# Optimization experiments

Hardware: AMD Instinct MI355X
Metric: run time of the kernel (lower is better)

Reference implementation:

```python
import jax, jax.numpy as jnp
import numpy as np

THETA = 10000.0
IDENTITY_WEIGHT = 0.5


def _rotary(x):
    """lucidrains RotaryEmbedding(dim=D//2).rotate_queries_or_keys(x).

    Rotates the first rot_dim = D//2 channels with interleaved pair rotation;
    remaining channels pass through unchanged. x: [B, S, D].
    """
    D = x.shape[-1]
    rot_dim = D // 2  # RotaryEmbedding(dim) rotates `dim` channels
    half = rot_dim // 2
    pos = jnp.arange(x.shape[-2], dtype=x.dtype)                      # [S]
    inv_freq = 1.0 / (THETA ** (jnp.arange(0, rot_dim, 2, dtype=x.dtype) / rot_dim))  # [half]
    freqs = pos[:, None] * inv_freq[None, :]                          # [S, half]
    freqs = jnp.repeat(freqs, 2, axis=-1)                             # [S, rot_dim] interleaved f0,f0,f1,f1,...
    cos, sin = jnp.cos(freqs), jnp.sin(freqs)
    xr, rest = x[..., :rot_dim], x[..., rot_dim:]
    x1, x2 = xr[..., 0::2], xr[..., 1::2]
    rot_half = jnp.stack([-x2, x1], axis=-1).reshape(xr.shape)        # interleaved rotate_half
    out = xr * cos + rot_half * sin
    return jnp.concatenate([out, rest], axis=-1)


def setup_inputs() -> dict:
    key = jax.random.key(0)
    kx, kw = jax.random.split(key)
    B, S, D = 4, 4096, 2048
    X = jax.random.normal(kx, (B, S, D), dtype=jnp.float32)
    W = jax.random.normal(kw, (D, 2 * D), dtype=jnp.float32) * (1.0 / np.sqrt(D))
    b = jnp.zeros((2 * D,), dtype=jnp.float32)
    return {"X": X, "W": W, "b": b}


def reference(X, W, b):
    D = X.shape[-1]
    KV = jnp.einsum('bsd,df->bsf', X, W) + b          # in_proj: [B, S, 2D]
    K, V = KV[..., :D], KV[..., D:]
    K, V = _rotary(K), _rotary(V)
    fm = jnp.cos                                       # feature_map
    A = jnp.sum(fm(K) * fm(V), axis=-2, keepdims=True)  # reduce over sequence -> [B, 1, D]
    A = (1.0 - IDENTITY_WEIGHT) * A + IDENTITY_WEIGHT
    return A * X
```

## Files before the change

### kernel.cpp

```cpp
#include <hip/hip_runtime.h>
#include <hip/hip_bf16.h>

typedef __attribute__((ext_vector_type(4)))  int   i32x4;
typedef __attribute__((ext_vector_type(8)))  int   i32x8;
typedef __attribute__((ext_vector_type(16))) float f32x16;

#define NEG_L2K (-0.025952563241307517f)

#define VMW(N) asm volatile("s_waitcnt vmcnt(" #N ")" ::: "memory")
#define SCHB() __builtin_amdgcn_sched_barrier(0)
#define SBAR() __builtin_amdgcn_s_barrier()

#define AS1 __attribute__((address_space(1)))
#define AS3 __attribute__((address_space(3)))

__device__ __forceinline__ unsigned int pk4_fp8(float a, float b, float c, float d) {
    unsigned int v = __builtin_amdgcn_cvt_pk_fp8_f32(a, b, 0, false);
    v = __builtin_amdgcn_cvt_pk_fp8_f32(c, d, v, true);
    return v;
}

__global__ __launch_bounds__(256) void prep_x_kernel(const float* __restrict__ X,
                                                     unsigned char* __restrict__ Xf,
                                                     float* __restrict__ A) {
    int g = blockIdx.x * 256 + threadIdx.x;
    if (g < 8192) A[g] = 0.0f;
    int tileid = g >> 9;
    int mtile  = tileid >> 5;
    int kt     = tileid & 31;
    int c      = g & 511;
    int s      = c >> 6;
    int lane   = c & 63;
    int row  = mtile * 128 + (s >> 1) * 32 + (lane & 31);
    int kcol = kt * 64 + (lane >> 5) * 32 + (s & 1) * 16;
    const float* src = X + (size_t)row * 2048 + kcol;
    float4 f0 = *(const float4*)(src);
    float4 f1 = *(const float4*)(src + 4);
    float4 f2 = *(const float4*)(src + 8);
    float4 f3 = *(const float4*)(src + 12);
    uint4 o;
    o.x = pk4_fp8(f0.x, f0.y, f0.z, f0.w);
    o.y = pk4_fp8(f1.x, f1.y, f1.z, f1.w);
    o.z = pk4_fp8(f2.x, f2.y, f2.z, f2.w);
    o.w = pk4_fp8(f3.x, f3.y, f3.z, f3.w);
    *(uint4*)(Xf + (size_t)g * 16) = o;
}

__global__ __launch_bounds__(256) void prep_w_kernel(const float* __restrict__ W,
                                                     unsigned char* __restrict__ Wf) {
    __shared__ unsigned char t[64][72];
    int f0 = blockIdx.x * 64;
    int k0 = blockIdx.y * 64;
    int tx = threadIdx.x & 63;
    int ty = threadIdx.x >> 6;
    for (int r = ty; r < 64; r += 4) {
        float w = W[(size_t)(k0 + r) * 4096 + f0 + tx] * 16.0f;
        t[r][tx] = (unsigned char)(__builtin_amdgcn_cvt_pk_fp8_f32(w, w, 0, false) & 0xFF);
    }
    __syncthreads();
    int c   = threadIdx.x;
    int il  = c & 31;
    int lh  = (c >> 5) & 1;
    int rd  = (c >> 6) & 1;
    int wcl = c >> 7;
    int col_l = wcl * 32 + il;
    int kl    = lh * 32 + rd * 16;
    int fh    = f0 & 2047;
    int KV    = f0 >> 11;
    int ntile = fh >> 7;
    int wcg   = ((fh >> 5) & 2) + wcl;
    union { unsigned char b[16]; uint4 v; } ob;
    #pragma unroll
    for (int b = 0; b < 16; ++b) ob.b[b] = t[kl + b][col_l];
    size_t base = ((((size_t)ntile * 32 + blockIdx.y) * 2 + KV) << 13)
                + (size_t)(((wcg * 2 + rd) * 64 + lh * 32 + il) << 4);
    *(uint4*)(Wf + base) = ob.v;
}

__global__ __launch_bounds__(256, 2) void gemm_acos_kernel(
    const unsigned char* __restrict__ Xf,
    const unsigned char* __restrict__ Wf,
    const float* __restrict__ bias,
    float* __restrict__ A)
{
    __shared__ __align__(16) unsigned char Als[2][8192];
    __shared__ __align__(16) unsigned char Kls[2][8192];
    __shared__ __align__(16) unsigned char Vls[2][8192];

    const int tid  = threadIdx.x;
    const int lane = tid & 63;
    const int wc   = tid >> 6;
    const int l31  = lane & 31;
    const int lh   = lane >> 5;

    const int orig  = blockIdx.x;
    const int wg    = (orig & 7) * 256 + (orig >> 3);
    const int mtile = wg & 127;
    const int ntile = wg >> 7;
    const int row0  = mtile * 128;
    const int n0    = ntile * 128;

    const unsigned char* XfT = Xf + ((size_t)(mtile * 32) << 13);
    const unsigned char* WfT = Wf + ((size_t)(ntile * 32) << 14);

    f32x16 accK[4] = {};
    f32x16 accV[4] = {};

    const int abase = lane * 16;
    const int bbase = (wc * 128 + lane) * 16;

    #define STAGE(T, NB)                                                                    \
        do {                                                                                \
            const unsigned char* ga = XfT + ((size_t)(T) << 13);                            \
            const unsigned char* gw = WfT + ((size_t)(T) << 14);                            \
            __builtin_amdgcn_global_load_lds((const AS1 void*)(ga + tid * 16),              \
                (AS3 void*)(Als[NB] + tid * 16), 16, 0, 0);                                 \
            __builtin_amdgcn_global_load_lds((const AS1 void*)(ga + 4096 + tid * 16),       \
                (AS3 void*)(Als[NB] + 4096 + tid * 16), 16, 0, 0);                          \
            __builtin_amdgcn_global_load_lds((const AS1 void*)(gw + tid * 16),              \
                (AS3 void*)(Kls[NB] + tid * 16), 16, 0, 0);                                 \
            __builtin_amdgcn_global_load_lds((const AS1 void*)(gw + 4096 + tid * 16),       \
                (AS3 void*)(Kls[NB] + 4096 + tid * 16), 16, 0, 0);                          \
            __builtin_amdgcn_global_load_lds((const AS1 void*)(gw + 8192 + tid * 16),       \
                (AS3 void*)(Vls[NB] + tid * 16), 16, 0, 0);                                 \
            __builtin_amdgcn_global_load_lds((const AS1 void*)(gw + 12288 + tid * 16),      \
                (AS3 void*)(Vls[NB] + 4096 + tid * 16), 16, 0, 0);                          \
        } while (0)

    STAGE(0, 0);

    #pragma unroll 1
    for (int it = 0; it < 16; ++it) {
        #pragma unroll
        for (int sub = 0; sub < 2; ++sub) {
            const int t = it * 2 + sub;
            const bool last = (t == 31);
            const unsigned char* As = Als[sub];
            const unsigned char* Ks = Kls[sub];
            const unsigned char* Vs = Vls[sub];

            if (!last) { STAGE(t + 1, sub ^ 1); VMW(6); } else { VMW(0); }
            SCHB();
            SBAR();

            i32x8 a8[4], bk8, bv8;
            #pragma unroll
            for (int mf = 0; mf < 4; ++mf) {
                i32x4 lo = *(const i32x4*)(As + abase + mf * 2048);
                i32x4 hi = *(const i32x4*)(As + abase + mf * 2048 + 1024);
                a8[mf] = __builtin_shufflevector(lo, hi, 0, 1, 2, 3, 4, 5, 6, 7);
            }
            {
                i32x4 lo = *(const i32x4*)(Ks + bbase);
                i32x4 hi = *(const i32x4*)(Ks + bbase + 1024);
                bk8 = __builtin_shufflevector(lo, hi, 0, 1, 2, 3, 4, 5, 6, 7);
            }
            __builtin_amdgcn_s_setprio(1);
            #pragma unroll
            for (int mf = 0; mf < 4; ++mf)
                accK[mf] = __builtin_amdgcn_mfma_scale_f32_32x32x64_f8f6f4(
                    a8[mf], bk8, accK[mf], 0, 0, 0, 0x7F7F7F7F, 0, 0x7B7B7B7B);
            __builtin_amdgcn_s_setprio(0);

            {
                i32x4 lo = *(const i32x4*)(Vs + bbase);
                i32x4 hi = *(const i32x4*)(Vs + bbase + 1024);
                bv8 = __builtin_shufflevector(lo, hi, 0, 1, 2, 3, 4, 5, 6, 7);
            }
            __builtin_amdgcn_s_setprio(1);
            #pragma unroll
            for (int mf = 0; mf < 4; ++mf)
                accV[mf] = __builtin_amdgcn_mfma_scale_f32_32x32x64_f8f6f4(
                    a8[mf], bv8, accV[mf], 0, 0, 0, 0x7F7F7F7F, 0, 0x7B7B7B7B);
            __builtin_amdgcn_s_setprio(0);
            SBAR();
        }
    }

    const int batch = row0 >> 12;
    const int c     = n0 + wc * 32 + l31;
    const float bK  = bias[c];
    const float bV  = bias[c + 2048];
    const bool rot  = (c < 1024);
    const float invf = exp2f((float)(c >> 1) * NEG_L2K);
    const float sgn  = (c & 1) ? 1.0f : -1.0f;
    const int sbase  = (row0 & 4095) + 4 * lh;

    float colsum = 0.0f;
    #pragma unroll
    for (int mf = 0; mf < 4; ++mf) {
        #pragma unroll
        for (int r = 0; r < 16; ++r) {
            const int srow = sbase + mf * 32 + (r & 3) + 8 * (r >> 2);
            float kv = accK[mf][r] + bK;
            float vv = accV[mf][r] + bV;
            float pk = __shfl_xor(kv, 1);
            float pv = __shfl_xor(vv, 1);
            float kr = kv, vr = vv;
            if (rot) {
                float sn, cs;
                __sincosf((float)srow * invf, &sn, &cs);
                float tt = sgn * sn;
                kr = kv * cs + pk * tt;
                vr = vv * cs + pv * tt;
            }
            colsum += __cosf(kr) * __cosf(vr);
        }
    }
    colsum += __shfl_xor(colsum, 32);
    if (lane < 32)
        atomicAdd(&A[batch * 2048 + c], colsum);
}

__global__ void scale_out_kernel(const float* __restrict__ X,
                                 const float* __restrict__ A,
                                 float* __restrict__ out, int n4) {
    int gid = blockIdx.x * blockDim.x + threadIdx.x;
    int stride = gridDim.x * blockDim.x;
    for (int i = gid; i < n4; i += stride) {
        int e0 = i * 4;
        int b  = e0 >> 23;
        int d  = e0 & 2047;
        float4 a4 = *(const float4*)(A + b * 2048 + d);
        float4 x4 = ((const float4*)X)[i];
        float4 o;
        o.x = (0.5f * a4.x + 0.5f) * x4.x;
        o.y = (0.5f * a4.y + 0.5f) * x4.y;
        o.z = (0.5f * a4.z + 0.5f) * x4.z;
        o.w = (0.5f * a4.w + 0.5f) * x4.w;
        ((float4*)out)[i] = o;
    }
}

extern "C" void kernel_launch(void* const* d_in, const int* in_sizes, int n_in,
                              void* d_out, int out_size, void* d_ws, size_t ws_size,
                              hipStream_t stream) {
    const float* X    = (const float*)d_in[0];
    const float* W    = (const float*)d_in[1];
    const float* bias = (const float*)d_in[2];
    float* out = (float*)d_out;

    const size_t szA  = 32768;
    const size_t szWf = (size_t)4096 * 2048;
    const size_t szXf = (size_t)16384 * 2048;

    char* ws = (char*)d_ws;
    float* A = (float*)ws;
    unsigned char* Wf;
    unsigned char* Xf;
    if (ws_size >= szA + szWf + szXf) {
        Wf = (unsigned char*)(ws + szA);
        Xf = (unsigned char*)(ws + szA + szWf);
    } else if (ws_size >= szA + szWf) {
        Wf = (unsigned char*)(ws + szA);
        Xf = (unsigned char*)d_out;
    } else {
        Xf = (unsigned char*)d_out;
        Wf = (unsigned char*)d_out + szXf;
    }

    prep_x_kernel<<<8192, 256, 0, stream>>>(X, Xf, A);
    prep_w_kernel<<<dim3(64, 32), 256, 0, stream>>>(W, Wf);
    gemm_acos_kernel<<<2048, 256, 0, stream>>>(Xf, Wf, bias, A);
    scale_out_kernel<<<2048, 256, 0, stream>>>(X, A, out, 16384 * 2048 / 4);
}
```

Measured before the change: 232.0 us.

## Split GEMM tile to 64 columns with separate K and V waves for occupancy

Halves the N tile per workgroup to 64 columns and launches twice as many blocks. Each pair of waves now computes only K or only V, which halves the accumulators per thread, and the launch bound is raised to three blocks per CU. The epilogue combines cos(K) and cos(V) by staging cos(K) in LDS, which adds a block-wide sync and some LDS traffic. The trade-off is that the A tile is now loaded twice as often overall.

```diff
diff --git a/kernel.cpp b/kernel.cpp
--- a/kernel.cpp
+++ b/kernel.cpp
@@ -77,54 +77,53 @@
     *(uint4*)(Wf + base) = ob.v;
 }
 
-__global__ __launch_bounds__(256, 2) void gemm_acos_kernel(
+__global__ __launch_bounds__(256, 3) void gemm_acos_kernel(
     const unsigned char* __restrict__ Xf,
     const unsigned char* __restrict__ Wf,
     const float* __restrict__ bias,
     float* __restrict__ A)
 {
-    __shared__ __align__(16) unsigned char Als[2][8192];
-    __shared__ __align__(16) unsigned char Kls[2][8192];
-    __shared__ __align__(16) unsigned char Vls[2][8192];
+    __shared__ __align__(16) unsigned char SMEM[32768];
+    unsigned char* Als0 = SMEM;
+    unsigned char* Kls0 = SMEM + 16384;
+    unsigned char* Vls0 = SMEM + 24576;
 
     const int tid  = threadIdx.x;
     const int lane = tid & 63;
-    const int wc   = tid >> 6;
+    const int wid  = tid >> 6;
+    const int kv   = wid >> 1;
+    const int ch   = wid & 1;
     const int l31  = lane & 31;
     const int lh   = lane >> 5;
 
     const int orig  = blockIdx.x;
-    const int wg    = (orig & 7) * 256 + (orig >> 3);
+    const int wg    = (orig & 7) * 512 + (orig >> 3);
     const int mtile = wg & 127;
-    const int ntile = wg >> 7;
+    const int nt64  = wg >> 7;
     const int row0  = mtile * 128;
-    const int n0    = ntile * 128;
+    const int n0    = nt64 * 64;
 
     const unsigned char* XfT = Xf + ((size_t)(mtile * 32) << 13);
-    const unsigned char* WfT = Wf + ((size_t)(ntile * 32) << 14);
-
-    f32x16 accK[4] = {};
-    f32x16 accV[4] = {};
+    const unsigned char* WfT = Wf + ((size_t)((nt64 >> 1) * 32) << 14);
+    const int subN = (nt64 & 1) * 4096;
+
+    f32x16 acc[4] = {};
 
     const int abase = lane * 16;
-    const int bbase = (wc * 128 + lane) * 16;
+    const int bbase = ch * 2048 + lane * 16;
 
     #define STAGE(T, NB)                                                                    \
         do {                                                                                \
             const unsigned char* ga = XfT + ((size_t)(T) << 13);                            \
-            const unsigned char* gw = WfT + ((size_t)(T) << 14);                            \
+            const unsigned char* gw = WfT + ((size_t)(T) << 14) + subN;                     \
             __builtin_amdgcn_global_load_lds((const AS1 void*)(ga + tid * 16),              \
-                (AS3 void*)(Als[NB] + tid * 16), 16, 0, 0);                                 \
+                (AS3 void*)(Als0 + (NB) * 8192 + tid * 16), 16, 0, 0);                      \
             __builtin_amdgcn_global_load_lds((const AS1 void*)(ga + 4096 + tid * 16),       \
-                (AS3 void*)(Als[NB] + 4096 + tid * 16), 16, 0, 0);                          \
+                (AS3 void*)(Als0 + (NB) * 8192 + 4096 + tid * 16), 16, 0, 0);               \
             __builtin_amdgcn_global_load_lds((const AS1 void*)(gw + tid * 16),              \
-                (AS3 void*)(Kls[NB] + tid * 16), 16, 0, 0);                                 \
-            __builtin_amdgcn_global_load_lds((const AS1 void*)(gw + 4096 + tid * 16),       \
-                (AS3 void*)(Kls[NB] + 4096 + tid * 16), 16, 0, 0);                          \
+                (AS3 void*)(Kls0 + (NB) * 4096 + tid * 16), 16, 0, 0);                      \
             __builtin_amdgcn_global_load_lds((const AS1 void*)(gw + 8192 + tid * 16),       \
-                (AS3 void*)(Vls[NB] + tid * 16), 16, 0, 0);                                 \
-            __builtin_amdgcn_global_load_lds((const AS1 void*)(gw + 12288 + tid * 16),      \
-                (AS3 void*)(Vls[NB] + 4096 + tid * 16), 16, 0, 0);                          \
+                (AS3 void*)(Vls0 + (NB) * 4096 + tid * 16), 16, 0, 0);                      \
         } while (0)
 
     STAGE(0, 0);
@@ -135,15 +134,14 @@
         for (int sub = 0; sub < 2; ++sub) {
             const int t = it * 2 + sub;
             const bool last = (t == 31);
-            const unsigned char* As = Als[sub];
-            const unsigned char* Ks = Kls[sub];
-            const unsigned char* Vs = Vls[sub];
-
-            if (!last) { STAGE(t + 1, sub ^ 1); VMW(6); } else { VMW(0); }
+            const unsigned char* As = Als0 + sub * 8192;
+            const unsigned char* Bs = (kv ? Vls0 : Kls0) + sub * 4096;
+
+            if (!last) { STAGE(t + 1, sub ^ 1); VMW(4); } else { VMW(0); }
             SCHB();
             SBAR();
 
-            i32x8 a8[4], bk8, bv8;
+            i32x8 a8[4], b8;
             #pragma unroll
             for (int mf = 0; mf < 4; ++mf) {
                 i32x4 lo = *(const i32x4*)(As + abase + mf * 2048);
@@ -151,65 +149,65 @@
                 a8[mf] = __builtin_shufflevector(lo, hi, 0, 1, 2, 3, 4, 5, 6, 7);
             }
             {
-                i32x4 lo = *(const i32x4*)(Ks + bbase);
-                i32x4 hi = *(const i32x4*)(Ks + bbase + 1024);
-                bk8 = __builtin_shufflevector(lo, hi, 0, 1, 2, 3, 4, 5, 6, 7);
+                i32x4 lo = *(const i32x4*)(Bs + bbase);
+                i32x4 hi = *(const i32x4*)(Bs + bbase + 1024);
+                b8 = __builtin_shufflevector(lo, hi, 0, 1, 2, 3, 4, 5, 6, 7);
             }
             __builtin_amdgcn_s_setprio(1);
             #pragma unroll
             for (int mf = 0; mf < 4; ++mf)
-                accK[mf] = __builtin_amdgcn_mfma_scale_f32_32x32x64_f8f6f4(
-                    a8[mf], bk8, accK[mf], 0, 0, 0, 0x7F7F7F7F, 0, 0x7B7B7B7B);
-            __builtin_amdgcn_s_setprio(0);
-
-            {
-                i32x4 lo = *(const i32x4*)(Vs + bbase);
-                i32x4 hi = *(const i32x4*)(Vs + bbase + 1024);
-                bv8 = __builtin_shufflevector(lo, hi, 0, 1, 2, 3, 4, 5, 6, 7);
-            }
-            __builtin_amdgcn_s_setprio(1);
-            #pragma unroll
-            for (int mf = 0; mf < 4; ++mf)
-                accV[mf] = __builtin_amdgcn_mfma_scale_f32_32x32x64_f8f6f4(
-                    a8[mf], bv8, accV[mf], 0, 0, 0, 0x7F7F7F7F, 0, 0x7B7B7B7B);
+                acc[mf] = __builtin_amdgcn_mfma_scale_f32_32x32x64_f8f6f4(
+                    a8[mf], b8, acc[mf], 0, 0, 0, 0x7F7F7F7F, 0, 0x7B7B7B7B);
             __builtin_amdgcn_s_setprio(0);
             SBAR();
         }
     }
 
     const int batch = row0 >> 12;
-    const int c     = n0 + wc * 32 + l31;
-    const float bK  = bias[c];
-    const float bV  = bias[c + 2048];
+    const int c     = n0 + ch * 32 + l31;
+    const float bb  = bias[c + kv * 2048];
     const bool rot  = (c < 1024);
     const float invf = exp2f((float)(c >> 1) * NEG_L2K);
     const float sgn  = (c & 1) ? 1.0f : -1.0f;
     const int sbase  = (row0 & 4095) + 4 * lh;
 
-    float colsum = 0.0f;
+    float* cosLds = (float*)SMEM;
+    __syncthreads();
+
+    float cs_arr[4][16];
     #pragma unroll
     for (int mf = 0; mf < 4; ++mf) {
         #pragma unroll
         for (int r = 0; r < 16; ++r) {
-            const int srow = sbase + mf * 32 + (r & 3) + 8 * (r >> 2);
-            float kv = accK[mf][r] + bK;
-            float vv = accV[mf][r] + bV;
-            float pk = __shfl_xor(kv, 1);
-            float pv = __shfl_xor(vv, 1);
-            float kr = kv, vr = vv;
+            const int rloc = mf * 32 + (r & 3) + 8 * (r >> 2) + 4 * lh;
+            float x  = acc[mf][r] + bb;
+            float px = __shfl_xor(x, 1);
+            float xr = x;
             if (rot) {
-                float sn, cs;
-                __sincosf((float)srow * invf, &sn, &cs);
-                float tt = sgn * sn;
-                kr = kv * cs + pk * tt;
-                vr = vv * cs + pv * tt;
-            }
-            colsum += __cosf(kr) * __cosf(vr);
+                float sn, cc;
+                __sincosf((float)(sbase - 4 * lh + rloc) * invf, &sn, &cc);
+                xr = x * cc + px * (sgn * sn);
+            }
+            cs_arr[mf][r] = __cosf(xr);
+            if (kv == 0)
+                cosLds[ch * 4096 + rloc * 32 + l31] = cs_arr[mf][r];
         }
     }
-    colsum += __shfl_xor(colsum, 32);
-    if (lane < 32)
-        atomicAdd(&A[batch * 2048 + c], colsum);
+    __syncthreads();
+    if (kv == 1) {
+        float colsum = 0.0f;
+        #pragma unroll
+        for (int mf = 0; mf < 4; ++mf) {
+            #pragma unroll
+            for (int r = 0; r < 16; ++r) {
+                const int rloc = mf * 32 + (r & 3) + 8 * (r >> 2) + 4 * lh;
+                colsum += cs_arr[mf][r] * cosLds[ch * 4096 + rloc * 32 + l31];
+            }
+        }
+        colsum += __shfl_xor(colsum, 32);
+        if (lane < 32)
+            atomicAdd(&A[batch * 2048 + c], colsum);
+    }
 }
 
 __global__ void scale_out_kernel(const float* __restrict__ X,
@@ -261,6 +259,6 @@
 
     prep_x_kernel<<<8192, 256, 0, stream>>>(X, Xf, A);
     prep_w_kernel<<<dim3(64, 32), 256, 0, stream>>>(W, Wf);
-    gemm_acos_kernel<<<2048, 256, 0, stream>>>(Xf, Wf, bias, A);
+    gemm_acos_kernel<<<4096, 256, 0, stream>>>(Xf, Wf, bias, A);
     scale_out_kernel<<<2048, 256, 0, stream>>>(X, A, out, 16384 * 2048 / 4);
 }
```

Result: slower. 269.9 us (+16.4%).

## Widen GEMM block tile to 256 output columns per K and V

Applied to the files above, without the earlier changes.

Each block now computes two adjacent 128-column N tiles, so each wave holds 2x the K and V accumulators and reuses each loaded A fragment across twice as many MFMAs. The grid halves to 1024 blocks, LDS per block grows to 80KB, and launch bounds drop to one block per CU's worth of occupancy. The intent is to cut the re-reading of X tiles from global memory and LDS per unit of compute, at the cost of higher register pressure, lower occupancy, and fewer blocks to balance across CUs.

```diff
diff --git a/kernel.cpp b/kernel.cpp
--- a/kernel.cpp
+++ b/kernel.cpp
@@ -77,54 +77,64 @@
     *(uint4*)(Wf + base) = ob.v;
 }
 
-__global__ __launch_bounds__(256, 2) void gemm_acos_kernel(
+__global__ __launch_bounds__(256, 1) void gemm_acos_kernel(
     const unsigned char* __restrict__ Xf,
     const unsigned char* __restrict__ Wf,
     const float* __restrict__ bias,
     float* __restrict__ A)
 {
     __shared__ __align__(16) unsigned char Als[2][8192];
-    __shared__ __align__(16) unsigned char Kls[2][8192];
-    __shared__ __align__(16) unsigned char Vls[2][8192];
+    __shared__ __align__(16) unsigned char Kls[2][16384];
+    __shared__ __align__(16) unsigned char Vls[2][16384];
 
     const int tid  = threadIdx.x;
     const int lane = tid & 63;
-    const int wc   = tid >> 6;
+    const int w    = tid >> 6;
     const int l31  = lane & 31;
     const int lh   = lane >> 5;
 
     const int orig  = blockIdx.x;
-    const int wg    = (orig & 7) * 256 + (orig >> 3);
+    const int wg    = (orig & 7) * 128 + (orig >> 3);
     const int mtile = wg & 127;
-    const int ntile = wg >> 7;
+    const int npair = wg >> 7;
     const int row0  = mtile * 128;
-    const int n0    = ntile * 128;
+    const int n0    = npair * 256;
 
     const unsigned char* XfT = Xf + ((size_t)(mtile * 32) << 13);
-    const unsigned char* WfT = Wf + ((size_t)(ntile * 32) << 14);
-
-    f32x16 accK[4] = {};
-    f32x16 accV[4] = {};
+    const unsigned char* W0  = Wf + ((size_t)(npair * 2) * 32 << 14);
+    const unsigned char* W1  = W0 + ((size_t)32 << 14);
+
+    f32x16 accK[4][2] = {};
+    f32x16 accV[4][2] = {};
 
     const int abase = lane * 16;
-    const int bbase = (wc * 128 + lane) * 16;
+    const int bbase = (w >> 1) * 8192 + (w & 1) * 4096 + lane * 16;
 
     #define STAGE(T, NB)                                                                    \
         do {                                                                                \
-            const unsigned char* ga = XfT + ((size_t)(T) << 13);                            \
-            const unsigned char* gw = WfT + ((size_t)(T) << 14);                            \
+            const unsigned char* ga  = XfT + ((size_t)(T) << 13);                           \
+            const unsigned char* gk0 = W0 + ((size_t)(T) << 14);                            \
+            const unsigned char* gk1 = W1 + ((size_t)(T) << 14);                            \
             __builtin_amdgcn_global_load_lds((const AS1 void*)(ga + tid * 16),              \
                 (AS3 void*)(Als[NB] + tid * 16), 16, 0, 0);                                 \
             __builtin_amdgcn_global_load_lds((const AS1 void*)(ga + 4096 + tid * 16),       \
                 (AS3 void*)(Als[NB] + 4096 + tid * 16), 16, 0, 0);                          \
-            __builtin_amdgcn_global_load_lds((const AS1 void*)(gw + tid * 16),              \
+            __builtin_amdgcn_global_load_lds((const AS1 void*)(gk0 + tid * 16),             \
                 (AS3 void*)(Kls[NB] + tid * 16), 16, 0, 0);                                 \
-            __builtin_amdgcn_global_load_lds((const AS1 void*)(gw + 4096 + tid * 16),       \
+            __builtin_amdgcn_global_load_lds((const AS1 void*)(gk0 + 4096 + tid * 16),      \
                 (AS3 void*)(Kls[NB] + 4096 + tid * 16), 16, 0, 0);                          \
-            __builtin_amdgcn_global_load_lds((const AS1 void*)(gw + 8192 + tid * 16),       \
+            __builtin_amdgcn_global_load_lds((const AS1 void*)(gk1 + tid * 16),             \
+                (AS3 void*)(Kls[NB] + 8192 + tid * 16), 16, 0, 0);                          \
+            __builtin_amdgcn_global_load_lds((const AS1 void*)(gk1 + 4096 + tid * 16),      \
+                (AS3 void*)(Kls[NB] + 12288 + tid * 16), 16, 0, 0);                         \
+            __builtin_amdgcn_global_load_lds((const AS1 void*)(gk0 + 8192 + tid * 16),      \
                 (AS3 void*)(Vls[NB] + tid * 16), 16, 0, 0);                                 \
-            __builtin_amdgcn_global_load_lds((const AS1 void*)(gw + 12288 + tid * 16),      \
+            __builtin_amdgcn_global_load_lds((const AS1 void*)(gk0 + 12288 + tid * 16),     \
                 (AS3 void*)(Vls[NB] + 4096 + tid * 16), 16, 0, 0);                          \
+            __builtin_amdgcn_global_load_lds((const AS1 void*)(gk1 + 8192 + tid * 16),      \
+                (AS3 void*)(Vls[NB] + 8192 + tid * 16), 16, 0, 0);                          \
+            __builtin_amdgcn_global_load_lds((const AS1 void*)(gk1 + 12288 + tid * 16),     \
+                (AS3 void*)(Vls[NB] + 12288 + tid * 16), 16, 0, 0);                         \
         } while (0)
 
     STAGE(0, 0);
@@ -139,77 +149,86 @@
             const unsigned char* Ks = Kls[sub];
             const unsigned char* Vs = Vls[sub];
 
-            if (!last) { STAGE(t + 1, sub ^ 1); VMW(6); } else { VMW(0); }
+            if (!last) { STAGE(t + 1, sub ^ 1); VMW(10); } else { VMW(0); }
             SCHB();
             SBAR();
 
-            i32x8 a8[4], bk8, bv8;
+            i32x8 a8[4], bk8[2], bv8[2];
             #pragma unroll
             for (int mf = 0; mf < 4; ++mf) {
                 i32x4 lo = *(const i32x4*)(As + abase + mf * 2048);
                 i32x4 hi = *(const i32x4*)(As + abase + mf * 2048 + 1024);
                 a8[mf] = __builtin_shufflevector(lo, hi, 0, 1, 2, 3, 4, 5, 6, 7);
             }
-            {
-                i32x4 lo = *(const i32x4*)(Ks + bbase);
-                i32x4 hi = *(const i32x4*)(Ks + bbase + 1024);
-                bk8 = __builtin_shufflevector(lo, hi, 0, 1, 2, 3, 4, 5, 6, 7);
+            #pragma unroll
+            for (int n = 0; n < 2; ++n) {
+                i32x4 lo = *(const i32x4*)(Ks + bbase + n * 2048);
+                i32x4 hi = *(const i32x4*)(Ks + bbase + n * 2048 + 1024);
+                bk8[n] = __builtin_shufflevector(lo, hi, 0, 1, 2, 3, 4, 5, 6, 7);
             }
             __builtin_amdgcn_s_setprio(1);
             #pragma unroll
             for (int mf = 0; mf < 4; ++mf)
-                accK[mf] = __builtin_amdgcn_mfma_scale_f32_32x32x64_f8f6f4(
-                    a8[mf], bk8, accK[mf], 0, 0, 0, 0x7F7F7F7F, 0, 0x7B7B7B7B);
+                #pragma unroll
+                for (int n = 0; n < 2; ++n)
+                    accK[mf][n] = __builtin_amdgcn_mfma_scale_f32_32x32x64_f8f6f4(
+                        a8[mf], bk8[n], accK[mf][n], 0, 0, 0, 0x7F7F7F7F, 0, 0x7B7B7B7B);
             __builtin_amdgcn_s_setprio(0);
 
-            {
-                i32x4 lo = *(const i32x4*)(Vs + bbase);
-                i32x4 hi = *(const i32x4*)(Vs + bbase + 1024);
-                bv8 = __builtin_shufflevector(lo, hi, 0, 1, 2, 3, 4, 5, 6, 7);
+            #pragma unroll
+            for (int n = 0; n < 2; ++n) {
+                i32x4 lo = *(const i32x4*)(Vs + bbase + n * 2048);
+                i32x4 hi = *(const i32x4*)(Vs + bbase + n * 2048 + 1024);
+                bv8[n] = __builtin_shufflevector(lo, hi, 0, 1, 2, 3, 4, 5, 6, 7);
             }
             __builtin_amdgcn_s_setprio(1);
             #pragma unroll
             for (int mf = 0; mf < 4; ++mf)
-                accV[mf] = __builtin_amdgcn_mfma_scale_f32_32x32x64_f8f6f4(
-                    a8[mf], bv8, accV[mf], 0, 0, 0, 0x7F7F7F7F, 0, 0x7B7B7B7B);
+                #pragma unroll
+                for (int n = 0; n < 2; ++n)
+                    accV[mf][n] = __builtin_amdgcn_mfma_scale_f32_32x32x64_f8f6f4(
+                        a8[mf], bv8[n], accV[mf][n], 0, 0, 0, 0x7F7F7F7F, 0, 0x7B7B7B7B);
             __builtin_amdgcn_s_setprio(0);
             SBAR();
         }
     }
 
     const int batch = row0 >> 12;
-    const int c     = n0 + wc * 32 + l31;
-    const float bK  = bias[c];
-    const float bV  = bias[c + 2048];
-    const bool rot  = (c < 1024);
-    const float invf = exp2f((float)(c >> 1) * NEG_L2K);
-    const float sgn  = (c & 1) ? 1.0f : -1.0f;
-    const int sbase  = (row0 & 4095) + 4 * lh;
-
-    float colsum = 0.0f;
+    const int sbase = (row0 & 4095) + 4 * lh;
+
     #pragma unroll
-    for (int mf = 0; mf < 4; ++mf) {
+    for (int n = 0; n < 2; ++n) {
+        const int c     = n0 + w * 64 + n * 32 + l31;
+        const float bK  = bias[c];
+        const float bV  = bias[c + 2048];
+        const bool rot  = (c < 1024);
+        const float invf = exp2f((float)(c >> 1) * NEG_L2K);
+        const float sgn  = (c & 1) ? 1.0f : -1.0f;
+        float colsum = 0.0f;
         #pragma unroll
-        for (int r = 0; r < 16; ++r) {
-            const int srow = sbase + mf * 32 + (r & 3) + 8 * (r >> 2);
-            float kv = accK[mf][r] + bK;
-            float vv = accV[mf][r] + bV;
-            float pk = __shfl_xor(kv, 1);
-            float pv = __shfl_xor(vv, 1);
-            float kr = kv, vr = vv;
-            if (rot) {
-                float sn, cs;
-                __sincosf((float)srow * invf, &sn, &cs);
-                float tt = sgn * sn;
-                kr = kv * cs + pk * tt;
-                vr = vv * cs + pv * tt;
-            }
-            colsum += __cosf(kr) * __cosf(vr);
+        for (int mf = 0; mf < 4; ++mf) {
+            #pragma unroll
+            for (int r = 0; r < 16; ++r) {
+                const int srow = sbase + mf * 32 + (r & 3) + 8 * (r >> 2);
+                float kv = accK[mf][n][r] + bK;
+                float vv = accV[mf][n][r] + bV;
+                float pk = __shfl_xor(kv, 1);
+                float pv = __shfl_xor(vv, 1);
+                float kr = kv, vr = vv;
+                if (rot) {
+                    float sn, cs;
+                    __sincosf((float)srow * invf, &sn, &cs);
+                    float tt = sgn * sn;
+                    kr = kv * cs + pk * tt;
+                    vr = vv * cs + pv * tt;
+                }
+                colsum += __cosf(kr) * __cosf(vr);
+            }
         }
-    }
-    colsum += __shfl_xor(colsum, 32);
-    if (lane < 32)
-        atomicAdd(&A[batch * 2048 + c], colsum);
+        colsum += __shfl_xor(colsum, 32);
+        if (lane < 32)
+            atomicAdd(&A[batch * 2048 + c], colsum);
+    }
 }
 
 __global__ void scale_out_kernel(const float* __restrict__ X,
@@ -261,6 +280,6 @@
 
     prep_x_kernel<<<8192, 256, 0, stream>>>(X, Xf, A);
     prep_w_kernel<<<dim3(64, 32), 256, 0, stream>>>(W, Wf);
-    gemm_acos_kernel<<<2048, 256, 0, stream>>>(Xf, Wf, bias, A);
+    gemm_acos_kernel<<<1024, 256, 0, stream>>>(Xf, Wf, bias, A);
     scale_out_kernel<<<2048, 256, 0, stream>>>(X, A, out, 16384 * 2048 / 4);
 }
```

Result: slower. 258.8 us (+11.5%).

## Triple-buffer LDS staging with two tiles in flight and single barrier

Applied to the files above, without the earlier changes.

Moves the GEMM main loop from double to triple LDS buffering. Two K-tiles are prefetched ahead with global_load_lds, and the second barrier per iteration is removed because a third buffer separates reads from writes. This gives loads more time to arrive and cuts synchronisation. In exchange LDS use grows from 48KB to 72KB per block, which may lower occupancy below the 2 blocks per CU requested by the launch bounds, and the loop is no longer manually unrolled, so buffer indexing uses modulo arithmetic.

```diff
diff --git a/kernel.cpp b/kernel.cpp
--- a/kernel.cpp
+++ b/kernel.cpp
@@ -83,9 +83,9 @@
     const float* __restrict__ bias,
     float* __restrict__ A)
 {
-    __shared__ __align__(16) unsigned char Als[2][8192];
-    __shared__ __align__(16) unsigned char Kls[2][8192];
-    __shared__ __align__(16) unsigned char Vls[2][8192];
+    __shared__ __align__(16) unsigned char Als0[3 * 8192];
+    __shared__ __align__(16) unsigned char Kls0[3 * 8192];
+    __shared__ __align__(16) unsigned char Vls0[3 * 8192];
 
     const int tid  = threadIdx.x;
     const int lane = tid & 63;
@@ -114,67 +114,65 @@
             const unsigned char* ga = XfT + ((size_t)(T) << 13);                            \
             const unsigned char* gw = WfT + ((size_t)(T) << 14);                            \
             __builtin_amdgcn_global_load_lds((const AS1 void*)(ga + tid * 16),              \
-                (AS3 void*)(Als[NB] + tid * 16), 16, 0, 0);                                 \
+                (AS3 void*)(Als0 + (NB) * 8192 + tid * 16), 16, 0, 0);                      \
             __builtin_amdgcn_global_load_lds((const AS1 void*)(ga + 4096 + tid * 16),       \
-                (AS3 void*)(Als[NB] + 4096 + tid * 16), 16, 0, 0);                          \
+                (AS3 void*)(Als0 + (NB) * 8192 + 4096 + tid * 16), 16, 0, 0);               \
             __builtin_amdgcn_global_load_lds((const AS1 void*)(gw + tid * 16),              \
-                (AS3 void*)(Kls[NB] + tid * 16), 16, 0, 0);                                 \
+                (AS3 void*)(Kls0 + (NB) * 8192 + tid * 16), 16, 0, 0);                      \
             __builtin_amdgcn_global_load_lds((const AS1 void*)(gw + 4096 + tid * 16),       \
-                (AS3 void*)(Kls[NB] + 4096 + tid * 16), 16, 0, 0);                          \
+                (AS3 void*)(Kls0 + (NB) * 8192 + 4096 + tid * 16), 16, 0, 0);               \
             __builtin_amdgcn_global_load_lds((const AS1 void*)(gw + 8192 + tid * 16),       \
-                (AS3 void*)(Vls[NB] + tid * 16), 16, 0, 0);                                 \
+                (AS3 void*)(Vls0 + (NB) * 8192 + tid * 16), 16, 0, 0);                      \
             __builtin_amdgcn_global_load_lds((const AS1 void*)(gw + 12288 + tid * 16),      \
-                (AS3 void*)(Vls[NB] + 4096 + tid * 16), 16, 0, 0);                          \
+                (AS3 void*)(Vls0 + (NB) * 8192 + 4096 + tid * 16), 16, 0, 0);               \
         } while (0)
 
     STAGE(0, 0);
+    STAGE(1, 1);
 
     #pragma unroll 1
-    for (int it = 0; it < 16; ++it) {
-        #pragma unroll
-        for (int sub = 0; sub < 2; ++sub) {
-            const int t = it * 2 + sub;
-            const bool last = (t == 31);
-            const unsigned char* As = Als[sub];
-            const unsigned char* Ks = Kls[sub];
-            const unsigned char* Vs = Vls[sub];
-
-            if (!last) { STAGE(t + 1, sub ^ 1); VMW(6); } else { VMW(0); }
-            SCHB();
-            SBAR();
-
-            i32x8 a8[4], bk8, bv8;
-            #pragma unroll
-            for (int mf = 0; mf < 4; ++mf) {
-                i32x4 lo = *(const i32x4*)(As + abase + mf * 2048);
-                i32x4 hi = *(const i32x4*)(As + abase + mf * 2048 + 1024);
-                a8[mf] = __builtin_shufflevector(lo, hi, 0, 1, 2, 3, 4, 5, 6, 7);
-            }
-            {
-                i32x4 lo = *(const i32x4*)(Ks + bbase);
-                i32x4 hi = *(const i32x4*)(Ks + bbase + 1024);
-                bk8 = __builtin_shufflevector(lo, hi, 0, 1, 2, 3, 4, 5, 6, 7);
-            }
-            __builtin_amdgcn_s_setprio(1);
-            #pragma unroll
-            for (int mf = 0; mf < 4; ++mf)
-                accK[mf] = __builtin_amdgcn_mfma_scale_f32_32x32x64_f8f6f4(
-                    a8[mf], bk8, accK[mf], 0, 0, 0, 0x7F7F7F7F, 0, 0x7B7B7B7B);
-            __builtin_amdgcn_s_setprio(0);
-
-            {
-                i32x4 lo = *(const i32x4*)(Vs + bbase);
-                i32x4 hi = *(const i32x4*)(Vs + bbase + 1024);
-                bv8 = __builtin_shufflevector(lo, hi, 0, 1, 2, 3, 4, 5, 6, 7);
-            }
-            __builtin_amdgcn_s_setprio(1);
-            #pragma unroll
-            for (int mf = 0; mf < 4; ++mf)
-                accV[mf] = __builtin_amdgcn_mfma_scale_f32_32x32x64_f8f6f4(
-                    a8[mf], bv8, accV[mf], 0, 0, 0, 0x7F7F7F7F, 0, 0x7B7B7B7B);
-            __builtin_amdgcn_s_setprio(0);
-            SBAR();
-        }
+    for (int t = 0; t < 32; ++t) {
+        const int cur = t % 3;
+        const unsigned char* As = Als0 + cur * 8192;
+        const unsigned char* Ks = Kls0 + cur * 8192;
+        const unsigned char* Vs = Vls0 + cur * 8192;
+
+        if (t < 31) { VMW(6); } else { VMW(0); }
+        SCHB();
+        SBAR();
+
+        if (t < 30) STAGE(t + 2, (t + 2) % 3);
+
+        i32x8 a8[4], bk8, bv8;
+        #pragma unroll
+        for (int mf = 0; mf < 4; ++mf) {
+            i32x4 lo = *(const i32x4*)(As + abase + mf * 2048);
+            i32x4 hi = *(const i32x4*)(As + abase + mf * 2048 + 1024);
+            a8[mf] = __builtin_shufflevector(lo, hi, 0, 1, 2, 3, 4, 5, 6, 7);
+        }
+        {
+            i32x4 lo = *(const i32x4*)(Ks + bbase);
+            i32x4 hi = *(const i32x4*)(Ks + bbase + 1024);
+            bk8 = __builtin_shufflevector(lo, hi, 0, 1, 2, 3, 4, 5, 6, 7);
+        }
+        __builtin_amdgcn_s_setprio(1);
+        #pragma unroll
+        for (int mf = 0; mf < 4; ++mf)
+            accK[mf] = __builtin_amdgcn_mfma_scale_f32_32x32x64_f8f6f4(
+                a8[mf], bk8, accK[mf], 0, 0, 0, 0x7F7F7F7F, 0, 0x7B7B7B7B);
+        __builtin_amdgcn_s_setprio(0);
+
+        {
+            i32x4 lo = *(const i32x4*)(Vs + bbase);
+            i32x4 hi = *(const i32x4*)(Vs + bbase + 1024);
+            bv8 = __builtin_shufflevector(lo, hi, 0, 1, 2, 3, 4, 5, 6, 7);
+        }
+        __builtin_amdgcn_s_setprio(1);
+        #pragma unroll
+        for (int mf = 0; mf < 4; ++mf)
+            accV[mf] = __builtin_amdgcn_mfma_scale_f32_32x32x64_f8f6f4(
+                a8[mf], bv8, accV[mf], 0, 0, 0, 0x7F7F7F7F, 0, 0x7B7B7B7B);
+        __builtin_amdgcn_s_setprio(0);
     }
 
     const int batch = row0 >> 12;
```

After: 242.1 us. +4.4%, slower.
